# Optimization experiments

Hardware: AMD Instinct MI355X
Metric: run time of the kernel (lower is better)

Reference implementation:

```python
import jax, jax.numpy as jnp
import numpy as np

B = 32768      # batch of graphs
H = 128        # hidden_channels
L = 3          # num message-passing layers
T = 3          # num_timesteps
NB, NJ = 1, 12 # base nodes, joint nodes
NN = NB + NJ   # 13 nodes per graph
OBS_W = 47     # obs features per timestep
BASE_IDX = np.array(list(range(9)) + [45, 46])   # 11 base features per timestep
JOINT_IDX = np.array(list(range(9, 45)))          # 36 joint features per timestep
BASE_F = T * len(BASE_IDX)                        # 33
JOINT_F = (len(JOINT_IDX) // NJ) * T              # 9

# fixed tree edges, both directions (24 edges per graph)
_n2n = np.array([[0, 0, 0, 0, 1, 2, 4, 5, 7, 8, 10, 11],
                 [1, 4, 7, 10, 2, 3, 5, 6, 8, 9, 11, 12]])
SRC = np.concatenate([_n2n[0], _n2n[1]])
DST = np.concatenate([_n2n[1], _n2n[0]])


def setup_inputs() -> dict:
    key = jax.random.key(0)
    ks = jax.random.split(key, 10)
    s = 0.05
    return {
        "obs": jax.random.normal(ks[0], (B, T * OBS_W), dtype=jnp.float32),
        "We_b": jax.random.normal(ks[1], (H, BASE_F), dtype=jnp.float32) * s,
        "be_b": jax.random.normal(ks[2], (H,), dtype=jnp.float32) * s,
        "We_j": jax.random.normal(ks[3], (H, JOINT_F), dtype=jnp.float32) * s,
        "be_j": jax.random.normal(ks[4], (H,), dtype=jnp.float32) * s,
        "W_rel": jax.random.normal(ks[5], (L, H, H), dtype=jnp.float32) * s,
        "W_root": jax.random.normal(ks[6], (L, H, H), dtype=jnp.float32) * s,
        "b_rel": jax.random.normal(ks[7], (L, H), dtype=jnp.float32) * s,
        "W_dec": jax.random.normal(ks[8], (1, H), dtype=jnp.float32) * s,
        "b_dec": jax.random.normal(ks[9], (1,), dtype=jnp.float32) * s,
        "src": jnp.asarray(SRC, dtype=jnp.int32),
        "dst": jnp.asarray(DST, dtype=jnp.int32),
    }


def reference(obs, We_b, be_b, We_j, be_j, W_rel, W_root, b_rel, W_dec, b_dec, src, dst):
    b = obs.shape[0]
    elu = jax.nn.elu
    # ---- obs -> per-node features ----
    obs3 = obs[:, :T * OBS_W].reshape(b, T, OBS_W)
    base_feat = obs3[:, :, BASE_IDX].reshape(b, NB, BASE_F)                 # [B,1,33]
    joint_feat = (obs3[:, :, JOINT_IDX]
                  .reshape(b, T, len(JOINT_IDX) // NJ, NJ)
                  .transpose(0, 3, 1, 2)
                  .reshape(b, NJ, JOINT_F))                                  # [B,12,9]
    # ---- encoders ----
    xb = elu(jnp.einsum('bnf,hf->bnh', base_feat, We_b) + be_b)
    xj = elu(jnp.einsum('bnf,hf->bnh', joint_feat, We_j) + be_j)
    x = jnp.concatenate([xb, xj], axis=1)                                    # [B,13,H]
    # ---- GraphConv layers: out = W_root x + W_rel (scatter_add of x_src at dst) + b ----
    for l in range(L):
        agg = jnp.zeros_like(x).at[:, dst].add(x[:, src])                    # [B,13,H]
        x = elu(jnp.einsum('bnh,oh->bno', agg, W_rel[l]) + b_rel[l]
                + jnp.einsum('bnh,oh->bno', x, W_root[l]))
    # ---- per-joint decoder ----
    out = jnp.einsum('bnh,oh->bno', x[:, NB:], W_dec) + b_dec                # [B,12,1]
    return out.reshape(b, NJ)
```

## Files before the change

### kernel.cpp

```cpp
#include <hip/hip_runtime.h>

#define H      128
#define OBSROW 141
#define GPB    16
#define NT     256

typedef __bf16 bf16x8 __attribute__((ext_vector_type(8)));
typedef float  f32x4  __attribute__((ext_vector_type(4)));

__device__ __forceinline__ float eluf(float v) {
    return v > 0.0f ? v : (__expf(v) - 1.0f);
}
__device__ __forceinline__ f32x4 mf(bf16x8 a, bf16x8 b, f32x4 c) {
    return __builtin_amdgcn_mfma_f32_16x16x32_bf16(a, b, c, 0, 0, 0);
}
__device__ __forceinline__ void store_pk4(unsigned short* dst, f32x4 a) {
    union { unsigned short u[4]; unsigned long long v; } pk;
    #pragma unroll
    for (int r = 0; r < 4; r++) {
        __bf16 b = (__bf16)eluf(a[r]);
        pk.u[r] = *(unsigned short*)&b;
    }
    *(unsigned long long*)dst = pk.v;
}

#define WS_ROOT 49152
#define WS_EB   98304
#define WS_EJ   106496
#define WS_TOT  110592

__global__ void convert_weights(const float* __restrict__ Wr, const float* __restrict__ Wo,
                                const float* __restrict__ Web, const float* __restrict__ Wej,
                                __bf16* __restrict__ ws) {
    const int i = blockIdx.x * 256 + threadIdx.x;
    if (i < WS_ROOT) {
        ws[i] = (__bf16)Wr[i];
    } else if (i < WS_EB) {
        ws[i] = (__bf16)Wo[i - WS_ROOT];
    } else if (i < WS_EJ) {
        const int j = i - WS_EB, o = j >> 6, f = j & 63;
        ws[i] = (__bf16)(f < 33 ? Web[o*33 + f] : 0.0f);
    } else if (i < WS_TOT) {
        const int j = i - WS_EJ, o = j >> 5, f = j & 31;
        ws[i] = (__bf16)(f < 9 ? Wej[o*9 + f] : 0.0f);
    }
}

#define G0U 19456

__launch_bounds__(NT, 3)
__global__ void gnn_fused(const float* __restrict__ obs,
                          const float* __restrict__ be_b, const float* __restrict__ be_j,
                          const float* __restrict__ b_rel,
                          const float* __restrict__ W_dec, const float* __restrict__ b_dec,
                          const __bf16* __restrict__ wsb,
                          float* __restrict__ out, int B)
{
    __shared__ __align__(16) unsigned short Xs[13*2048];

    const int tid  = threadIdx.x;
    const int wave = tid >> 6;
    const int lane = tid & 63;
    const int q    = lane >> 4;
    const int c    = lane & 15;
    const int g0   = blockIdx.x * GPB;

    static constexpr int ODEG[13]    = {4,2,2,1,2,2,1,2,2,1,2,2,1};
    static constexpr int ODST[13][4] = {
        {1,4,7,10},{0,2,0,0},{1,3,0,0},{2,0,0,0},{0,5,0,0},{4,6,0,0},{5,0,0,0},
        {0,8,0,0},{7,9,0,0},{8,0,0,0},{0,11,0,0},{10,12,0,0},{11,0,0,0}};

    const int hcs0 = wave*4 + (q>>1);
    const int wofs = c*8 + (q&1)*4;

    {
        float* raw = (float*)Xs;
        for (int i = tid; i < GPB*OBSROW; i += NT) {
            const int g = i / OBSROW;
            raw[i] = ((g0 + g) < B) ? obs[(g0+g)*OBSROW + (i - g*OBSROW)] : 0.0f;
        }
    }
    __syncthreads();

    {
        const float* raw = (const float*)Xs;
        for (int s = tid; s < 6144; s += NT) {
            const int jj = s >> 9, rem = s & 511;
            const int fc = rem >> 7, g = (rem >> 3) & 15, hi = rem & 7;
            const int f = fc*8 + hi;
            float v = 0.0f;
            if (f < 9)
                v = raw[g*OBSROW + (f/3)*47 + 9 + (f%3)*12 + jj];
            *(__bf16*)&Xs[G0U + s] = (__bf16)v;
        }
        for (int s = tid; s < 1024; s += NT) {
            const int fc = s >> 7, rem = s & 127, g = rem >> 3, hi = rem & 7;
            const int f = fc*8 + hi;
            float v = 0.0f;
            if (f < 33) {
                const int tt = f / 11, i2 = f % 11;
                v = raw[g*OBSROW + tt*47 + (i2 < 9 ? i2 : 36 + i2)];
            }
            *(__bf16*)&Xs[G0U + 6144 + s] = (__bf16)v;
        }
    }
    __syncthreads();

    {
        const int orow = wave*32 + c;
        const bf16x8 a0 = *(const bf16x8*)&Xs[G0U + 6144 + q*128 + c*8];
        const bf16x8 a1 = *(const bf16x8*)&Xs[G0U + 6144 + 512 + q*128 + c*8];
        #pragma unroll
        for (int s = 0; s < 2; s++) {
            const bf16x8 u0 = *(const bf16x8*)(wsb + WS_EB + (orow + s*16)*64 + q*8);
            const bf16x8 u1 = *(const bf16x8*)(wsb + WS_EB + (orow + s*16)*64 + 32 + q*8);
            const float4 b4 = *(const float4*)&be_b[wave*32 + s*16 + q*4];
            f32x4 acc = {b4.x, b4.y, b4.z, b4.w};
            acc = mf(u0, a0, acc);
            acc = mf(u1, a1, acc);
            store_pk4(&Xs[(hcs0 + s*2)*128 + wofs], acc);
        }
        bf16x8 uj[2];
        f32x4 bias[2];
        #pragma unroll
        for (int s = 0; s < 2; s++) {
            uj[s] = *(const bf16x8*)(wsb + WS_EJ + (orow + s*16)*32 + q*8);
            const float4 b4 = *(const float4*)&be_j[wave*32 + s*16 + q*4];
            bias[s] = (f32x4){b4.x, b4.y, b4.z, b4.w};
        }
        f32x4 dacc[2][4];
        #pragma unroll
        for (int jj = 0; jj < 12; jj++) {
            const bf16x8 a = *(const bf16x8*)&Xs[G0U + jj*512 + q*128 + c*8];
            #pragma unroll
            for (int s = 0; s < 2; s++) {
                f32x4 acc = bias[s];
                acc = mf(uj[s], a, acc);
                if (jj < 8)
                    store_pk4(&Xs[(1+jj)*2048 + (hcs0 + s*2)*128 + wofs], acc);
                else
                    dacc[s][jj-8] = acc;
            }
        }
        __syncthreads();
        #pragma unroll
        for (int t = 0; t < 4; t++) {
            store_pk4(&Xs[(9+t)*2048 +  hcs0     *128 + wofs], dacc[0][t]);
            store_pk4(&Xs[(9+t)*2048 + (hcs0+2)  *128 + wofs], dacc[1][t]);
        }
    }
    __syncthreads();

    const unsigned short* xb_base = Xs + q*128 + c*8;
    #pragma unroll 1
    for (int l = 0; l < 3; l++) {
        const __bf16* wr = wsb + l*16384;
        const __bf16* wo = wsb + WS_ROOT + l*16384;
        bf16x8 Wr[2][4], Wt[2][4];
        #pragma unroll
        for (int s = 0; s < 2; s++) {
            const int row = (wave*32 + s*16 + c)*128 + q*8;
            #pragma unroll
            for (int ks = 0; ks < 4; ks++) {
                Wr[s][ks] = *(const bf16x8*)(wr + row + ks*32);
                Wt[s][ks] = *(const bf16x8*)(wo + row + ks*32);
            }
        }
        f32x4 acc[13][2];
        #pragma unroll
        for (int s = 0; s < 2; s++) {
            const float4 b4 = *(const float4*)&b_rel[l*H + wave*32 + s*16 + q*4];
            const f32x4 bias = {b4.x, b4.y, b4.z, b4.w};
            #pragma unroll
            for (int n = 0; n < 13; n++) acc[n][s] = bias;
        }
        #pragma unroll
        for (int n = 0; n < 13; n++) {
            bf16x8 xb[4];
            #pragma unroll
            for (int ks = 0; ks < 4; ks++)
                xb[ks] = *(const bf16x8*)(xb_base + n*2048 + ks*512);
            f32x4 y0 = {0.f,0.f,0.f,0.f}, y1 = {0.f,0.f,0.f,0.f};
            #pragma unroll
            for (int ks = 0; ks < 4; ks++) {
                acc[n][0] = mf(Wt[0][ks], xb[ks], acc[n][0]);
                acc[n][1] = mf(Wt[1][ks], xb[ks], acc[n][1]);
                y0 = mf(Wr[0][ks], xb[ks], y0);
                y1 = mf(Wr[1][ks], xb[ks], y1);
            }
            #pragma unroll
            for (int e = 0; e < 4; e++)
                if (e < ODEG[n]) {
                    acc[ODST[n][e]][0] += y0;
                    acc[ODST[n][e]][1] += y1;
                }
        }
        __syncthreads();
        #pragma unroll
        for (int n = 0; n < 13; n++) {
            store_pk4(&Xs[n*2048 +  hcs0     *128 + wofs], acc[n][0]);
            store_pk4(&Xs[n*2048 + (hcs0 + 2)*128 + wofs], acc[n][1]);
        }
        __syncthreads();
    }

    {
        const unsigned short* xdec = Xs + q*512 + c*8;
        float wd[32];
        #pragma unroll
        for (int i4 = 0; i4 < 8; i4++) {
            const float4 wv = *(const float4*)&W_dec[q*32 + i4*4];
            wd[i4*4+0] = wv.x; wd[i4*4+1] = wv.y; wd[i4*4+2] = wv.z; wd[i4*4+3] = wv.w;
        }
        const float bd = b_dec[0];
        for (int j = wave; j < 12; j += 4) {
            float s = 0.0f;
            #pragma unroll
            for (int hq = 0; hq < 4; hq++) {
                const bf16x8 xv = *(const bf16x8*)(xdec + (j+1)*2048 + hq*128);
                #pragma unroll
                for (int hi2 = 0; hi2 < 8; hi2++)
                    s += (float)xv[hi2] * wd[hq*8 + hi2];
            }
            s += __shfl_xor(s, 16);
            s += __shfl_xor(s, 32);
            if (q == 0 && (g0 + c) < B)
                out[(g0 + c)*12 + j] = s + bd;
        }
    }
}

extern "C" void kernel_launch(void* const* d_in, const int* in_sizes, int n_in,
                              void* d_out, int out_size, void* d_ws, size_t ws_size,
                              hipStream_t stream) {
    const float* obs   = (const float*)d_in[0];
    const float* We_b  = (const float*)d_in[1];
    const float* be_b  = (const float*)d_in[2];
    const float* We_j  = (const float*)d_in[3];
    const float* be_j  = (const float*)d_in[4];
    const float* W_rel = (const float*)d_in[5];
    const float* W_root= (const float*)d_in[6];
    const float* b_rel = (const float*)d_in[7];
    const float* W_dec = (const float*)d_in[8];
    const float* b_dec = (const float*)d_in[9];
    float* out = (float*)d_out;
    __bf16* wsb = (__bf16*)d_ws;

    const int B = in_sizes[0] / OBSROW;
    convert_weights<<<(WS_TOT + 255) / 256, 256, 0, stream>>>(W_rel, W_root, We_b, We_j, wsb);
    const int blocks = (B + GPB - 1) / GPB;
    gnn_fused<<<blocks, NT, 0, stream>>>(obs, be_b, be_j, b_rel, W_dec, b_dec,
                                         wsb, out, B);
}
```

Measured before the change: 217.0 us.

## Prefetch layer weights early, apply relational MFMA per edge, fuse decoder into last layer

Layer 0 weights are now loaded before the first barrier, and the next layer's weights are prefetched while the current layer's results are written to LDS. The separate relational product plus vector adds per edge is replaced by MFMAs that accumulate straight into each destination node. This uses more matrix instructions but fewer live registers, and the K loop is split into two halves. The last layer skips node 0 and fuses ELU and the decoder dot product, reducing per-wave partial sums through LDS. Launch bounds drop from 3 to 2 waves per SIMD to give the compiler more registers.

```diff
diff --git a/kernel.cpp b/kernel.cpp
--- a/kernel.cpp
+++ b/kernel.cpp
@@ -48,7 +48,7 @@
 
 #define G0U 19456
 
-__launch_bounds__(NT, 3)
+__launch_bounds__(NT, 2)
 __global__ void gnn_fused(const float* __restrict__ obs,
                           const float* __restrict__ be_b, const float* __restrict__ be_j,
                           const float* __restrict__ b_rel,
@@ -72,6 +72,8 @@
 
     const int hcs0 = wave*4 + (q>>1);
     const int wofs = c*8 + (q&1)*4;
+    const int rb0 = (wave*32 + c)*128 + q*8;
+    const int rb1 = (wave*32 + 16 + c)*128 + q*8;
 
     {
         float* raw = (float*)Xs;
@@ -79,6 +81,14 @@
             const int g = i / OBSROW;
             raw[i] = ((g0 + g) < B) ? obs[(g0+g)*OBSROW + (i - g*OBSROW)] : 0.0f;
         }
+    }
+    bf16x8 Wt[2][4], Wr[2][4];
+    #pragma unroll
+    for (int ks = 0; ks < 4; ks++) {
+        Wt[0][ks] = *(const bf16x8*)(wsb + WS_ROOT + rb0 + ks*32);
+        Wt[1][ks] = *(const bf16x8*)(wsb + WS_ROOT + rb1 + ks*32);
+        Wr[0][ks] = *(const bf16x8*)(wsb + rb0 + ks*32);
+        Wr[1][ks] = *(const bf16x8*)(wsb + rb1 + ks*32);
     }
     __syncthreads();
 
@@ -153,19 +163,7 @@
 
     const unsigned short* xb_base = Xs + q*128 + c*8;
     #pragma unroll 1
-    for (int l = 0; l < 3; l++) {
-        const __bf16* wr = wsb + l*16384;
-        const __bf16* wo = wsb + WS_ROOT + l*16384;
-        bf16x8 Wr[2][4], Wt[2][4];
-        #pragma unroll
-        for (int s = 0; s < 2; s++) {
-            const int row = (wave*32 + s*16 + c)*128 + q*8;
-            #pragma unroll
-            for (int ks = 0; ks < 4; ks++) {
-                Wr[s][ks] = *(const bf16x8*)(wr + row + ks*32);
-                Wt[s][ks] = *(const bf16x8*)(wo + row + ks*32);
-            }
-        }
+    for (int l = 0; l < 2; l++) {
         f32x4 acc[13][2];
         #pragma unroll
         for (int s = 0; s < 2; s++) {
@@ -175,25 +173,27 @@
             for (int n = 0; n < 13; n++) acc[n][s] = bias;
         }
         #pragma unroll
-        for (int n = 0; n < 13; n++) {
-            bf16x8 xb[4];
-            #pragma unroll
-            for (int ks = 0; ks < 4; ks++)
-                xb[ks] = *(const bf16x8*)(xb_base + n*2048 + ks*512);
-            f32x4 y0 = {0.f,0.f,0.f,0.f}, y1 = {0.f,0.f,0.f,0.f};
-            #pragma unroll
-            for (int ks = 0; ks < 4; ks++) {
-                acc[n][0] = mf(Wt[0][ks], xb[ks], acc[n][0]);
-                acc[n][1] = mf(Wt[1][ks], xb[ks], acc[n][1]);
-                y0 = mf(Wr[0][ks], xb[ks], y0);
-                y1 = mf(Wr[1][ks], xb[ks], y1);
+        for (int h = 0; h < 2; h++) {
+            const unsigned short* xh = xb_base + 2*h*512;
+            #pragma unroll
+            for (int n = 0; n < 13; n++) {
+                const bf16x8 xa0 = *(const bf16x8*)(xh + n*2048);
+                const bf16x8 xa1 = *(const bf16x8*)(xh + n*2048 + 512);
+                acc[n][0] = mf(Wt[0][2*h  ], xa0, acc[n][0]);
+                acc[n][0] = mf(Wt[0][2*h+1], xa1, acc[n][0]);
+                acc[n][1] = mf(Wt[1][2*h  ], xa0, acc[n][1]);
+                acc[n][1] = mf(Wt[1][2*h+1], xa1, acc[n][1]);
+                #pragma unroll
+                for (int e = 0; e < 4; e++) {
+                    if (e < ODEG[n]) {
+                        const int d = ODST[n][e];
+                        acc[d][0] = mf(Wr[0][2*h  ], xa0, acc[d][0]);
+                        acc[d][0] = mf(Wr[0][2*h+1], xa1, acc[d][0]);
+                        acc[d][1] = mf(Wr[1][2*h  ], xa0, acc[d][1]);
+                        acc[d][1] = mf(Wr[1][2*h+1], xa1, acc[d][1]);
+                    }
+                }
             }
-            #pragma unroll
-            for (int e = 0; e < 4; e++)
-                if (e < ODEG[n]) {
-                    acc[ODST[n][e]][0] += y0;
-                    acc[ODST[n][e]][1] += y1;
-                }
         }
         __syncthreads();
         #pragma unroll
@@ -201,31 +201,85 @@
             store_pk4(&Xs[n*2048 +  hcs0     *128 + wofs], acc[n][0]);
             store_pk4(&Xs[n*2048 + (hcs0 + 2)*128 + wofs], acc[n][1]);
         }
+        #pragma unroll
+        for (int ks = 0; ks < 4; ks++) {
+            Wt[0][ks] = *(const bf16x8*)(wsb + WS_ROOT + (l+1)*16384 + rb0 + ks*32);
+            Wt[1][ks] = *(const bf16x8*)(wsb + WS_ROOT + (l+1)*16384 + rb1 + ks*32);
+            Wr[0][ks] = *(const bf16x8*)(wsb + (l+1)*16384 + rb0 + ks*32);
+            Wr[1][ks] = *(const bf16x8*)(wsb + (l+1)*16384 + rb1 + ks*32);
+        }
         __syncthreads();
     }
 
     {
-        const unsigned short* xdec = Xs + q*512 + c*8;
-        float wd[32];
-        #pragma unroll
-        for (int i4 = 0; i4 < 8; i4++) {
-            const float4 wv = *(const float4*)&W_dec[q*32 + i4*4];
-            wd[i4*4+0] = wv.x; wd[i4*4+1] = wv.y; wd[i4*4+2] = wv.z; wd[i4*4+3] = wv.w;
-        }
-        const float bd = b_dec[0];
-        for (int j = wave; j < 12; j += 4) {
-            float s = 0.0f;
-            #pragma unroll
-            for (int hq = 0; hq < 4; hq++) {
-                const bf16x8 xv = *(const bf16x8*)(xdec + (j+1)*2048 + hq*128);
+        f32x4 acc[13][2];
+        #pragma unroll
+        for (int s = 0; s < 2; s++) {
+            const float4 b4 = *(const float4*)&b_rel[2*H + wave*32 + s*16 + q*4];
+            const f32x4 bias = {b4.x, b4.y, b4.z, b4.w};
+            #pragma unroll
+            for (int n = 0; n < 13; n++) acc[n][s] = bias;
+        }
+        #pragma unroll
+        for (int h = 0; h < 2; h++) {
+            const unsigned short* xh = xb_base + 2*h*512;
+            #pragma unroll
+            for (int n = 0; n < 13; n++) {
+                const bf16x8 xa0 = *(const bf16x8*)(xh + n*2048);
+                const bf16x8 xa1 = *(const bf16x8*)(xh + n*2048 + 512);
+                if (n != 0) {
+                    acc[n][0] = mf(Wt[0][2*h  ], xa0, acc[n][0]);
+                    acc[n][0] = mf(Wt[0][2*h+1], xa1, acc[n][0]);
+                    acc[n][1] = mf(Wt[1][2*h  ], xa0, acc[n][1]);
+                    acc[n][1] = mf(Wt[1][2*h+1], xa1, acc[n][1]);
+                }
                 #pragma unroll
-                for (int hi2 = 0; hi2 < 8; hi2++)
-                    s += (float)xv[hi2] * wd[hq*8 + hi2];
+                for (int e = 0; e < 4; e++) {
+                    if (e < ODEG[n]) {
+                        const int d = ODST[n][e];
+                        if (d == 0) continue;
+                        acc[d][0] = mf(Wr[0][2*h  ], xa0, acc[d][0]);
+                        acc[d][0] = mf(Wr[0][2*h+1], xa1, acc[d][0]);
+                        acc[d][1] = mf(Wr[1][2*h  ], xa0, acc[d][1]);
+                        acc[d][1] = mf(Wr[1][2*h+1], xa1, acc[d][1]);
+                    }
+                }
             }
-            s += __shfl_xor(s, 16);
-            s += __shfl_xor(s, 32);
-            if (q == 0 && (g0 + c) < B)
-                out[(g0 + c)*12 + j] = s + bd;
+        }
+        __syncthreads();
+
+        float wd[2][4];
+        #pragma unroll
+        for (int s = 0; s < 2; s++) {
+            const float4 w4 = *(const float4*)&W_dec[wave*32 + s*16 + q*4];
+            wd[s][0] = w4.x; wd[s][1] = w4.y; wd[s][2] = w4.z; wd[s][3] = w4.w;
+        }
+        float* part = (float*)&Xs[G0U];
+        float p[12];
+        #pragma unroll
+        for (int j = 0; j < 12; j++) {
+            float pp = 0.0f;
+            #pragma unroll
+            for (int s = 0; s < 2; s++)
+                #pragma unroll
+                for (int r = 0; r < 4; r++)
+                    pp += eluf(acc[j+1][s][r]) * wd[s][r];
+            pp += __shfl_xor(pp, 16);
+            pp += __shfl_xor(pp, 32);
+            p[j] = pp;
+        }
+        if (q == 0) {
+            #pragma unroll
+            for (int j = 0; j < 12; j++)
+                part[wave*192 + j*16 + c] = p[j];
+        }
+        __syncthreads();
+        if (tid < 192) {
+            const int c2 = tid / 12, j2 = tid - c2*12;
+            const float ssum = part[      j2*16 + c2] + part[192 + j2*16 + c2]
+                             + part[384 + j2*16 + c2] + part[576 + j2*16 + c2];
+            if ((g0 + c2) < B)
+                out[(g0 + c2)*12 + j2] = ssum + b_dec[0];
         }
     }
 }
```

Result: faster. 207.0 us (-4.6%).
